# Optimization experiments

Measured on AMD Instinct MI355X. Metric: run time of the kernel, lower is better.

## Reference

```python
import jax, jax.numpy as jnp
import numpy as np

B, D3, L, H, O, E, GH = 4096, 288, 32, 512, 96, 8, 128


def _init_linear(key, out_dim, in_dim):
    kw, kb = jax.random.split(key)
    bound = 1.0 / np.sqrt(in_dim)
    W = jax.random.uniform(kw, (out_dim, in_dim), jnp.float32, -bound, bound)
    b = jax.random.uniform(kb, (out_dim,), jnp.float32, -bound, bound)
    return W, b


def setup_inputs() -> dict:
    key = jax.random.key(0)
    ks = jax.random.split(key, 12)
    x = jax.random.normal(ks[0], (B, D3), jnp.float32)
    z = jax.random.normal(ks[1], (B, L), jnp.float32)
    # per-expert weights, stacked on leading expert axis [E, out, in]
    def expert_stack(k, out_dim, in_dim):
        Ws, bs = [], []
        for i in range(E):
            Wi, bi = _init_linear(jax.random.fold_in(k, i), out_dim, in_dim)
            Ws.append(Wi); bs.append(bi)
        return jnp.stack(Ws), jnp.stack(bs)
    W0, b0 = expert_stack(ks[2], H, D3 + L)
    W1, b1 = expert_stack(ks[3], H, H + L)
    W2, b2 = expert_stack(ks[4], H, H + L)
    W3, b3 = expert_stack(ks[5], O, H)
    gW1, gb1 = _init_linear(ks[6], GH, D3 + L)
    gW2, gb2 = _init_linear(ks[7], GH, GH)
    gW3, gb3 = _init_linear(ks[8], E, GH)
    return {"x": x, "z": z, "W0": W0, "b0": b0, "W1": W1, "b1": b1,
            "W2": W2, "b2": b2, "W3": W3, "b3": b3,
            "gW1": gW1, "gb1": gb1, "gW2": gW2, "gb2": gb2,
            "gW3": gW3, "gb3": gb3}


def _gating(x, z, gW1, gb1, gW2, gb2, gW3, gb3):
    h = jnp.concatenate([x, z], axis=1)
    h = jax.nn.elu(h @ gW1.T + gb1)
    h = jax.nn.elu(h @ gW2.T + gb2)
    return jax.nn.softmax(h @ gW3.T + gb3, axis=-1)  # [B, E]


def _blended_linear(g, W, b, h):
    # Original: materializes sum_e g[b,e] * W_e -> [B,out,in], then bmm.
    # Mathematically identical linear form: sum_e g[b,e] * (W_e h_b + b_e).
    return jnp.einsum('be,eoi,bi->bo', g, W, h) + g @ b


def reference(x, z, W0, b0, W1, b1, W2, b2, W3, b3,
              gW1, gb1, gW2, gb2, gW3, gb3):
    g = _gating(x, z, gW1, gb1, gW2, gb2, gW3, gb3)  # [B, E]
    # dropout p=0.0 (eval) -> identity
    h = jax.nn.elu(_blended_linear(g, W0, b0, jnp.concatenate([x, z], axis=1)))
    h = jax.nn.elu(_blended_linear(g, W1, b1, jnp.concatenate([h, z], axis=1)))
    h = jax.nn.elu(_blended_linear(g, W2, b2, jnp.concatenate([h, z], axis=1)))
    out = _blended_linear(g, W3, b3, h)
    return out  # [B, O]
```

## Files before the change

kernel.cpp:

```cpp
#include <hip/hip_runtime.h>
#include <hip/hip_fp16.h>

typedef _Float16 half8 __attribute__((ext_vector_type(8)));
typedef _Float16 half4 __attribute__((ext_vector_type(4)));
typedef float floatx4 __attribute__((ext_vector_type(4)));

__device__ __forceinline__ void async_ld16(const void* g, void* l) {
    __builtin_amdgcn_global_load_lds(
        (const __attribute__((address_space(1))) char*)g,
        (__attribute__((address_space(3))) char*)l, 16, 0, 0);
}

__device__ __forceinline__ float elu_f(float v) {
    return v > 0.f ? v : (__expf(v) - 1.f);
}

__device__ __forceinline__ half4 cvt4(const float* src, int j4) {
    float4 f = ((const float4*)src)[j4];
    half4 h; h.x = (_Float16)f.x; h.y = (_Float16)f.y;
    h.z = (_Float16)f.z; h.w = (_Float16)f.w; return h;
}

__launch_bounds__(256)
__global__ void convert_all(const float* __restrict__ x, const float* __restrict__ z,
                            const float* __restrict__ W0, const float* __restrict__ W1,
                            const float* __restrict__ W2, const float* __restrict__ W3,
                            const float* __restrict__ gW1, const float* __restrict__ gW2,
                            const float* __restrict__ gW3,
                            _Float16* __restrict__ X0,
                            _Float16* __restrict__ h0, _Float16* __restrict__ h1,
                            _Float16* __restrict__ h2,
                            _Float16* __restrict__ Wc0, _Float16* __restrict__ Wc1,
                            _Float16* __restrict__ Wc2, _Float16* __restrict__ Wc3,
                            _Float16* __restrict__ gW1c, _Float16* __restrict__ gW2c,
                            _Float16* __restrict__ gW3c)
{
    const int S0 = 294912;
    const int S1 = 32768;
    const int S2 = 327680;
    const int S3 = 589824;
    const int S4 = 589824;
    const int S5 = 98304;
    const int S6 = 196608;
    const int S7 = 10240;
    const int S8 = 4096;
    const int TOTAL = S0 + S1 + S2 + S3 + S4 + S5 + S6 + S7 + S8 + 256;
    const half4 hz = {};

    for (int i = blockIdx.x * blockDim.x + threadIdx.x; i < TOTAL;
         i += gridDim.x * blockDim.x) {
        int j = i;
        if (j < S0) {
            int r = j / 72, c = j - r * 72;
            *(half4*)(X0 + r * 320 + c * 4) = cvt4(x, j);
            continue;
        }
        j -= S0;
        if (j < S1) {
            int r = j / 8, c = j - r * 8;
            *(half4*)(X0 + r * 320 + 288 + c * 4) = cvt4(z, j);
            continue;
        }
        j -= S1;
        if (j < S2) { *(half4*)(Wc0 + j * 4) = cvt4(W0, j); continue; }
        j -= S2;
        if (j < S3) {
            int r = j / 144, c = j - r * 144;
            *(half4*)(Wc1 + r * 576 + c * 4) = (c < 136) ? cvt4(W1, r * 136 + c) : hz;
            continue;
        }
        j -= S3;
        if (j < S4) {
            int r = j / 144, c = j - r * 144;
            *(half4*)(Wc2 + r * 576 + c * 4) = (c < 136) ? cvt4(W2, r * 136 + c) : hz;
            continue;
        }
        j -= S4;
        if (j < S5) { *(half4*)(Wc3 + j * 4) = cvt4(W3, j); continue; }
        j -= S5;
        if (j < S6) {
            int buf = j >> 16;
            int r2 = j & 65535;
            int row = r2 >> 4, c = r2 & 15;
            _Float16* h = (buf == 0) ? h0 : ((buf == 1) ? h1 : h2);
            *(half4*)(h + row * 576 + 512 + c * 4) = (c < 8) ? cvt4(z, row * 8 + c) : hz;
            continue;
        }
        j -= S6;
        if (j < S7) { *(half4*)(gW1c + j * 4) = cvt4(gW1, j); continue; }
        j -= S7;
        if (j < S8) { *(half4*)(gW2c + j * 4) = cvt4(gW2, j); continue; }
        j -= S8;
        *(half4*)(gW3c + j * 4) = cvt4(gW3, j);
    }
}

__launch_bounds__(256)
__global__ void gating_fast(const _Float16* __restrict__ X0,
                            const _Float16* __restrict__ gW1c,
                            const _Float16* __restrict__ gW2c,
                            const _Float16* __restrict__ gW3c,
                            const float* __restrict__ gb1,
                            const float* __restrict__ gb2,
                            const float* __restrict__ gb3,
                            float* __restrict__ g)
{
    __shared__ _Float16 Tbuf[4 * 16 * 136];

    const int tid = threadIdx.x;
    const int l = tid & 63;
    const int w = tid >> 6;
    const int quad = l >> 4;
    const int mi = l & 15;
    const int kq = quad * 8;
    const int mrow = (blockIdx.x * 4 + w) * 16;

    _Float16* T = Tbuf + w * (16 * 136);
    const _Float16* arow = X0 + (size_t)(mrow + mi) * 320;

    floatx4 acc1[8] = {};
    half8 a_nxt = *(const half8*)(arow + kq);
#pragma unroll
    for (int kc = 0; kc < 10; kc++) {
        const int k0 = kc * 32;
        half8 a = a_nxt;
        if (kc < 9) a_nxt = *(const half8*)(arow + k0 + 32 + kq);
#pragma unroll
        for (int t = 0; t < 8; t++) {
            half8 b = *(const half8*)(gW1c + (size_t)(t * 16 + mi) * 320 + k0 + kq);
            acc1[t] = __builtin_amdgcn_mfma_f32_16x16x32_f16(a, b, acc1[t], 0, 0, 0);
        }
    }
#pragma unroll
    for (int t = 0; t < 8; t++) {
        const int n = t * 16 + mi;
        const float bn = gb1[n];
#pragma unroll
        for (int r = 0; r < 4; r++)
            T[(quad * 4 + r) * 136 + n] = (_Float16)elu_f(acc1[t][r] + bn);
    }

    floatx4 acc2[8] = {};
#pragma unroll
    for (int kc = 0; kc < 4; kc++) {
        const int k0 = kc * 32;
        half8 a = *(const half8*)(T + mi * 136 + k0 + kq);
#pragma unroll
        for (int t = 0; t < 8; t++) {
            half8 b = *(const half8*)(gW2c + (size_t)(t * 16 + mi) * 128 + k0 + kq);
            acc2[t] = __builtin_amdgcn_mfma_f32_16x16x32_f16(a, b, acc2[t], 0, 0, 0);
        }
    }
#pragma unroll
    for (int t = 0; t < 8; t++) {
        const int n = t * 16 + mi;
        const float bn = gb2[n];
#pragma unroll
        for (int r = 0; r < 4; r++)
            T[(quad * 4 + r) * 136 + n] = (_Float16)elu_f(acc2[t][r] + bn);
    }

    floatx4 acc3 = {};
#pragma unroll
    for (int kc = 0; kc < 4; kc++) {
        const int k0 = kc * 32;
        half8 a = *(const half8*)(T + mi * 136 + k0 + kq);
        half8 b = (mi < 8) ? *(const half8*)(gW3c + (size_t)mi * 128 + k0 + kq) : half8{};
        acc3 = __builtin_amdgcn_mfma_f32_16x16x32_f16(a, b, acc3, 0, 0, 0);
    }
    const float gb = gb3[mi & 7];
#pragma unroll
    for (int r = 0; r < 4; r++) {
        float logit = acc3[r] + gb;
        float mx = logit;
        mx = fmaxf(mx, __shfl_xor(mx, 1));
        mx = fmaxf(mx, __shfl_xor(mx, 2));
        mx = fmaxf(mx, __shfl_xor(mx, 4));
        float e = __expf(logit - mx);
        float s = e;
        s += __shfl_xor(s, 1);
        s += __shfl_xor(s, 2);
        s += __shfl_xor(s, 4);
        if (mi < 8)
            g[(size_t)(mrow + quad * 4 + r) * 8 + mi] = e / s;
    }
}

template <bool ELU_ACT, bool SWZ, typename OUT_T>
__launch_bounds__(512, 4)
__global__ void blend256(const _Float16* __restrict__ A, int lda,
                         const _Float16* __restrict__ W, int ldw,
                         int Hdim, int K,
                         const float* __restrict__ g,
                         const float* __restrict__ bias,
                         OUT_T* __restrict__ out, int ldo)
{
    __shared__ __align__(16) char smem_raw[49152];
    _Float16* sA = (_Float16*)smem_raw;
    _Float16* sB = (_Float16*)(smem_raw + 32768);
    float* sredf = (float*)smem_raw;
    __shared__ _Float16 sg[256][8];
    __shared__ float sbias[8][16];

    const int tid = threadIdx.x;
    const int l = tid & 63;
    const int w = tid >> 6;
    const int wm = w >> 1, wn = w & 1;

    int by, bx;
    if (SWZ) {
        const int id = blockIdx.x;
        const int r = id & 7, q = id >> 3;
        by = (r >> 1) * 4 + (q & 3);
        bx = (r & 1) * 16 + (q >> 2);
    } else {
        const int id = blockIdx.x;
        by = id / 6;
        bx = id - by * 6;
    }
    const int o0 = bx * 16;
    const int m0 = by * 256;

    for (int t = tid; t < 256 * 8; t += 512)
        sg[t >> 3][t & 7] = (_Float16)g[(size_t)(m0 + (t >> 3)) * 8 + (t & 7)];
    if (tid < 128)
        sbias[tid >> 4][tid & 15] = bias[(tid >> 4) * Hdim + o0 + (tid & 15)];

    const int lr = l >> 3;
    const int lc = l & 7;
    const int swz = lc ^ lr;

    const _Float16* gAp = A + (size_t)(m0 + w * 32 + lr) * lda + swz * 8;
    _Float16* const lAp = sA + w * 2048;
    const _Float16* gBp = W + ((size_t)w * Hdim + o0 + lr) * ldw + swz * 8;
    _Float16* const lBp = sB + w * 1024;

    const int mi = l & 15, quad = l >> 4;
    const int cswz = mi & 7;
    const _Float16* const rAb = sA + (wm * 64 + mi) * 64;
    const _Float16* const rBb = sB + (wn * 64 + mi) * 64;

    floatx4 acc[4][4] = {};

    for (int k0 = 0; k0 < K; k0 += 64) {
        __syncthreads();
        {
            const _Float16* ga = gAp + k0;
#pragma unroll
            for (int c = 0; c < 4; c++)
                async_ld16(ga + (size_t)c * 8 * lda, lAp + c * 512);
            const _Float16* gb = gBp + k0;
#pragma unroll
            for (int c = 0; c < 2; c++)
                async_ld16(gb + (size_t)c * 8 * ldw, lBp + c * 512);
        }
        __syncthreads();
#pragma unroll
        for (int h = 0; h < 2; h++) {
            const int off = ((h * 4 + quad) ^ cswz) * 8;
            half8 af[4], bf[4];
#pragma unroll
            for (int i = 0; i < 4; i++) af[i] = *(const half8*)(rAb + i * 1024 + off);
#pragma unroll
            for (int j = 0; j < 4; j++) bf[j] = *(const half8*)(rBb + j * 1024 + off);
#pragma unroll
            for (int i = 0; i < 4; i++)
#pragma unroll
                for (int j = 0; j < 4; j++)
                    acc[i][j] = __builtin_amdgcn_mfma_f32_16x16x32_f16(af[i], bf[j], acc[i][j], 0, 0, 0);
        }
    }

    float p[4][4];
#pragma unroll
    for (int i = 0; i < 4; i++)
#pragma unroll
        for (int r = 0; r < 4; r++) {
            const int mloc = wm * 64 + i * 16 + quad * 4 + r;
            float s = 0.f;
#pragma unroll
            for (int j = 0; j < 4; j++) {
                const int e = wn * 4 + j;
                s += (float)sg[mloc][e] * (acc[i][j][r] + sbias[e][mi]);
            }
            p[i][r] = s;
        }

    __syncthreads();
    if (wn == 0) {
#pragma unroll
        for (int i = 0; i < 4; i++)
#pragma unroll
            for (int r = 0; r < 4; r++)
                sredf[(wm * 64 + i * 16 + quad * 4 + r) * 17 + mi] = p[i][r];
    }
    __syncthreads();
    if (wn == 1) {
#pragma unroll
        for (int i = 0; i < 4; i++)
#pragma unroll
            for (int r = 0; r < 4; r++) {
                const int mrel = wm * 64 + i * 16 + quad * 4 + r;
                float v = p[i][r] + sredf[mrel * 17 + mi];
                if (ELU_ACT) v = elu_f(v);
                out[(size_t)(m0 + mrel) * ldo + o0 + mi] = (OUT_T)v;
            }
    }
}

extern "C" void kernel_launch(void* const* d_in, const int* in_sizes, int n_in,
                              void* d_out, int out_size, void* d_ws, size_t ws_size,
                              hipStream_t stream)
{
    (void)in_sizes; (void)n_in; (void)out_size; (void)ws_size;
    const float* x   = (const float*)d_in[0];
    const float* z   = (const float*)d_in[1];
    const float* W0  = (const float*)d_in[2];
    const float* b0  = (const float*)d_in[3];
    const float* W1  = (const float*)d_in[4];
    const float* b1  = (const float*)d_in[5];
    const float* W2  = (const float*)d_in[6];
    const float* b2  = (const float*)d_in[7];
    const float* W3  = (const float*)d_in[8];
    const float* b3  = (const float*)d_in[9];
    const float* gW1 = (const float*)d_in[10];
    const float* gb1 = (const float*)d_in[11];
    const float* gW2 = (const float*)d_in[12];
    const float* gb2 = (const float*)d_in[13];
    const float* gW3 = (const float*)d_in[14];
    const float* gb3 = (const float*)d_in[15];

    char* p = (char*)d_ws;
    auto alloc = [&](size_t n) { char* r = p; p += (n + 255) & ~(size_t)255; return r; };
    _Float16* X0   = (_Float16*)alloc((size_t)4096 * 320 * 2);
    _Float16* h0   = (_Float16*)alloc((size_t)4096 * 576 * 2);
    _Float16* h1   = (_Float16*)alloc((size_t)4096 * 576 * 2);
    _Float16* h2   = (_Float16*)alloc((size_t)4096 * 576 * 2);
    _Float16* Wc0  = (_Float16*)alloc((size_t)8 * 512 * 320 * 2);
    _Float16* Wc1  = (_Float16*)alloc((size_t)8 * 512 * 576 * 2);
    _Float16* Wc2  = (_Float16*)alloc((size_t)8 * 512 * 576 * 2);
    _Float16* Wc3  = (_Float16*)alloc((size_t)8 * 96 * 512 * 2);
    _Float16* gW1c = (_Float16*)alloc((size_t)128 * 320 * 2);
    _Float16* gW2c = (_Float16*)alloc((size_t)128 * 128 * 2);
    _Float16* gW3c = (_Float16*)alloc((size_t)8 * 128 * 2);
    float*    g    = (float*)alloc((size_t)4096 * 8 * 4);

    convert_all<<<1024, 256, 0, stream>>>(x, z, W0, W1, W2, W3, gW1, gW2, gW3,
                                          X0, h0, h1, h2, Wc0, Wc1, Wc2, Wc3,
                                          gW1c, gW2c, gW3c);

    gating_fast<<<64, 256, 0, stream>>>(X0, gW1c, gW2c, gW3c, gb1, gb2, gb3, g);

    blend256<true, true, _Float16><<<512, 512, 0, stream>>>(X0, 320, Wc0, 320, 512, 320, g, b0, h0, 576);
    blend256<true, true, _Float16><<<512, 512, 0, stream>>>(h0, 576, Wc1, 576, 512, 576, g, b1, h1, 576);
    blend256<true, true, _Float16><<<512, 512, 0, stream>>>(h1, 576, Wc2, 576, 512, 576, g, b2, h2, 576);
    blend256<false, false, float><<<96, 512, 0, stream>>>(h2, 576, Wc3, 512, 96, 512, g, b3, (float*)d_out, 96);
}
```

Baseline: 189.1 us.

## Overlap weight conversion with gating and read B fragments directly from global

The expert weight fp32->fp16 conversion moves out of the first convert kernel into extra blocks of the gating kernel, so it runs alongside gating. The light convert kernel now handles only activations, z padding and gating weights. Separately, the blend GEMM stops staging weight tiles in LDS and loads the B fragments straight from global memory, which shrinks shared memory and drops the async B loads. The direct global B loads may be less coalesced and add latency inside the MFMA loop.

```diff
diff --git a/kernel.cpp b/kernel.cpp
--- a/kernel.cpp
+++ b/kernel.cpp
@@ -22,29 +22,21 @@
 }
 
 __launch_bounds__(256)
-__global__ void convert_all(const float* __restrict__ x, const float* __restrict__ z,
-                            const float* __restrict__ W0, const float* __restrict__ W1,
-                            const float* __restrict__ W2, const float* __restrict__ W3,
-                            const float* __restrict__ gW1, const float* __restrict__ gW2,
-                            const float* __restrict__ gW3,
-                            _Float16* __restrict__ X0,
-                            _Float16* __restrict__ h0, _Float16* __restrict__ h1,
-                            _Float16* __restrict__ h2,
-                            _Float16* __restrict__ Wc0, _Float16* __restrict__ Wc1,
-                            _Float16* __restrict__ Wc2, _Float16* __restrict__ Wc3,
-                            _Float16* __restrict__ gW1c, _Float16* __restrict__ gW2c,
-                            _Float16* __restrict__ gW3c)
+__global__ void convert_light(const float* __restrict__ x, const float* __restrict__ z,
+                              const float* __restrict__ gW1, const float* __restrict__ gW2,
+                              const float* __restrict__ gW3,
+                              _Float16* __restrict__ X0,
+                              _Float16* __restrict__ h0, _Float16* __restrict__ h1,
+                              _Float16* __restrict__ h2,
+                              _Float16* __restrict__ gW1c, _Float16* __restrict__ gW2c,
+                              _Float16* __restrict__ gW3c)
 {
     const int S0 = 294912;
     const int S1 = 32768;
-    const int S2 = 327680;
-    const int S3 = 589824;
-    const int S4 = 589824;
-    const int S5 = 98304;
     const int S6 = 196608;
     const int S7 = 10240;
     const int S8 = 4096;
-    const int TOTAL = S0 + S1 + S2 + S3 + S4 + S5 + S6 + S7 + S8 + 256;
+    const int TOTAL = S0 + S1 + S6 + S7 + S8 + 256;
     const half4 hz = {};
 
     for (int i = blockIdx.x * blockDim.x + threadIdx.x; i < TOTAL;
@@ -62,22 +54,6 @@
             continue;
         }
         j -= S1;
-        if (j < S2) { *(half4*)(Wc0 + j * 4) = cvt4(W0, j); continue; }
-        j -= S2;
-        if (j < S3) {
-            int r = j / 144, c = j - r * 144;
-            *(half4*)(Wc1 + r * 576 + c * 4) = (c < 136) ? cvt4(W1, r * 136 + c) : hz;
-            continue;
-        }
-        j -= S3;
-        if (j < S4) {
-            int r = j / 144, c = j - r * 144;
-            *(half4*)(Wc2 + r * 576 + c * 4) = (c < 136) ? cvt4(W2, r * 136 + c) : hz;
-            continue;
-        }
-        j -= S4;
-        if (j < S5) { *(half4*)(Wc3 + j * 4) = cvt4(W3, j); continue; }
-        j -= S5;
         if (j < S6) {
             int buf = j >> 16;
             int r2 = j & 65535;
@@ -96,18 +72,53 @@
 }
 
 __launch_bounds__(256)
-__global__ void gating_fast(const _Float16* __restrict__ X0,
-                            const _Float16* __restrict__ gW1c,
-                            const _Float16* __restrict__ gW2c,
-                            const _Float16* __restrict__ gW3c,
-                            const float* __restrict__ gb1,
-                            const float* __restrict__ gb2,
-                            const float* __restrict__ gb3,
-                            float* __restrict__ g)
+__global__ void gating_convW(const _Float16* __restrict__ X0,
+                             const _Float16* __restrict__ gW1c,
+                             const _Float16* __restrict__ gW2c,
+                             const _Float16* __restrict__ gW3c,
+                             const float* __restrict__ gb1,
+                             const float* __restrict__ gb2,
+                             const float* __restrict__ gb3,
+                             float* __restrict__ g,
+                             const float* __restrict__ W0, const float* __restrict__ W1,
+                             const float* __restrict__ W2, const float* __restrict__ W3,
+                             _Float16* __restrict__ Wc0, _Float16* __restrict__ Wc1,
+                             _Float16* __restrict__ Wc2, _Float16* __restrict__ Wc3)
 {
+    const int tid = threadIdx.x;
+
+    if (blockIdx.x >= 64) {
+        const int S2 = 327680;
+        const int S3 = 589824;
+        const int S4 = 589824;
+        const int S5 = 98304;
+        const int TOTAL = S2 + S3 + S4 + S5;
+        const int nb = gridDim.x - 64;
+        const half4 hz = {};
+        for (int i = (blockIdx.x - 64) * blockDim.x + tid; i < TOTAL;
+             i += nb * blockDim.x) {
+            int j = i;
+            if (j < S2) { *(half4*)(Wc0 + j * 4) = cvt4(W0, j); continue; }
+            j -= S2;
+            if (j < S3) {
+                int r = j / 144, c = j - r * 144;
+                *(half4*)(Wc1 + r * 576 + c * 4) = (c < 136) ? cvt4(W1, r * 136 + c) : hz;
+                continue;
+            }
+            j -= S3;
+            if (j < S4) {
+                int r = j / 144, c = j - r * 144;
+                *(half4*)(Wc2 + r * 576 + c * 4) = (c < 136) ? cvt4(W2, r * 136 + c) : hz;
+                continue;
+            }
+            j -= S4;
+            *(half4*)(Wc3 + j * 4) = cvt4(W3, j);
+        }
+        return;
+    }
+
     __shared__ _Float16 Tbuf[4 * 16 * 136];
 
-    const int tid = threadIdx.x;
     const int l = tid & 63;
     const int w = tid >> 6;
     const int quad = l >> 4;
@@ -195,9 +206,8 @@
                          const float* __restrict__ bias,
                          OUT_T* __restrict__ out, int ldo)
 {
-    __shared__ __align__(16) char smem_raw[49152];
+    __shared__ __align__(16) char smem_raw[32768];
     _Float16* sA = (_Float16*)smem_raw;
-    _Float16* sB = (_Float16*)(smem_raw + 32768);
     float* sredf = (float*)smem_raw;
     __shared__ _Float16 sg[256][8];
     __shared__ float sbias[8][16];
@@ -229,16 +239,16 @@
     const int lr = l >> 3;
     const int lc = l & 7;
     const int swz = lc ^ lr;
-
     const _Float16* gAp = A + (size_t)(m0 + w * 32 + lr) * lda + swz * 8;
     _Float16* const lAp = sA + w * 2048;
-    const _Float16* gBp = W + ((size_t)w * Hdim + o0 + lr) * ldw + swz * 8;
-    _Float16* const lBp = sB + w * 1024;
 
     const int mi = l & 15, quad = l >> 4;
     const int cswz = mi & 7;
     const _Float16* const rAb = sA + (wm * 64 + mi) * 64;
-    const _Float16* const rBb = sB + (wn * 64 + mi) * 64;
+    const _Float16* gB[4];
+#pragma unroll
+    for (int j = 0; j < 4; j++)
+        gB[j] = W + ((size_t)(wn * 4 + j) * Hdim + o0 + mi) * ldw + quad * 8;
 
     floatx4 acc[4][4] = {};
 
@@ -249,10 +259,6 @@
 #pragma unroll
             for (int c = 0; c < 4; c++)
                 async_ld16(ga + (size_t)c * 8 * lda, lAp + c * 512);
-            const _Float16* gb = gBp + k0;
-#pragma unroll
-            for (int c = 0; c < 2; c++)
-                async_ld16(gb + (size_t)c * 8 * ldw, lBp + c * 512);
         }
         __syncthreads();
 #pragma unroll
@@ -262,7 +268,7 @@
 #pragma unroll
             for (int i = 0; i < 4; i++) af[i] = *(const half8*)(rAb + i * 1024 + off);
 #pragma unroll
-            for (int j = 0; j < 4; j++) bf[j] = *(const half8*)(rBb + j * 1024 + off);
+            for (int j = 0; j < 4; j++) bf[j] = *(const half8*)(gB[j] + k0 + h * 32);
 #pragma unroll
             for (int i = 0; i < 4; i++)
 #pragma unroll
@@ -345,11 +351,11 @@
     _Float16* gW3c = (_Float16*)alloc((size_t)8 * 128 * 2);
     float*    g    = (float*)alloc((size_t)4096 * 8 * 4);
 
-    convert_all<<<1024, 256, 0, stream>>>(x, z, W0, W1, W2, W3, gW1, gW2, gW3,
-                                          X0, h0, h1, h2, Wc0, Wc1, Wc2, Wc3,
-                                          gW1c, gW2c, gW3c);
-
-    gating_fast<<<64, 256, 0, stream>>>(X0, gW1c, gW2c, gW3c, gb1, gb2, gb3, g);
+    convert_light<<<512, 256, 0, stream>>>(x, z, gW1, gW2, gW3,
+                                           X0, h0, h1, h2, gW1c, gW2c, gW3c);
+
+    gating_convW<<<1024, 256, 0, stream>>>(X0, gW1c, gW2c, gW3c, gb1, gb2, gb3, g,
+                                           W0, W1, W2, W3, Wc0, Wc1, Wc2, Wc3);
 
     blend256<true, true, _Float16><<<512, 512, 0, stream>>>(X0, 320, Wc0, 320, 512, 320, g, b0, h0, 576);
     blend256<true, true, _Float16><<<512, 512, 0, stream>>>(h0, 576, Wc1, 576, 512, 576, g, b1, h1, 576);
```

Measured after the change: 259.4 us. 1.37x slower.
